# Optimization experiments

Hardware: AMD Instinct MI355X
Metric: run time of the kernel (lower is better)

## Reference

```python
import jax, jax.numpy as jnp
import numpy as np

D = 512   # word_dim
H = 4     # heads
NEG = -1.0e9


def setup_inputs() -> dict:
    key = jax.random.key(0)
    ks = jax.random.split(key, 9)
    B, N, K = 4, 1024, 32
    neibor_embedding = jax.random.normal(ks[0], (B, N, K, D), dtype=jnp.float32)
    x = jax.random.normal(ks[1], (B, N, D), dtype=jnp.float32)
    mask = jax.random.randint(ks[2], (B, N, K), 0, 2, dtype=jnp.int32)
    s = 1.0 / np.sqrt(D)
    Wq = jax.random.normal(ks[3], (D, D), dtype=jnp.float32) * s
    bq = jax.random.normal(ks[4], (D,), dtype=jnp.float32) * s
    Wk = jax.random.normal(ks[5], (D, D), dtype=jnp.float32) * s
    bk = jax.random.normal(ks[6], (D,), dtype=jnp.float32) * s
    Wv = jax.random.normal(ks[7], (D, D), dtype=jnp.float32) * s
    bv = jax.random.normal(ks[8], (D,), dtype=jnp.float32) * s
    return {"neibor_embedding": neibor_embedding, "mask": mask, "x": x,
            "Wq": Wq, "bq": bq, "Wk": Wk, "bk": bk, "Wv": Wv, "bv": bv}


def reference(neibor_embedding, mask, x, Wq, bq, Wk, bk, Wv, bv):
    B, N, K, Dm = neibor_embedding.shape
    dh = Dm // H
    # torch Linear: y = x @ W.T + b
    q = x @ Wq.T + bq                        # [B, N, D]
    k = neibor_embedding @ Wk.T + bk         # [B, N, K, D]
    v = neibor_embedding @ Wv.T + bv         # [B, N, K, D]
    q = q.reshape(B, N, H, dh)
    k = k.reshape(B, N, K, H, dh)
    v = v.reshape(B, N, K, H, dh)
    # broadcast q*k sum over head_dim -> scores [B, N, H, K] (no 1/sqrt(d) scaling, per source)
    scores = jnp.einsum('bnhd,bnkhd->bnhk', q, k)
    m = (mask[:, :, None, :] == 0)           # [B, N, 1, K] broadcasts over heads
    scores = jnp.where(m, NEG, scores)
    attn = jax.nn.softmax(scores, axis=3)    # [B, N, H, K]
    vec = jnp.einsum('bnhk,bnkhd->bnhd', attn, v)  # [B, N, H, dh]
    return vec.reshape(B, N, Dm)
```

## Files before the change

### kernel.cpp

```cpp
#include <hip/hip_runtime.h>

#define DD   512
#define KK_N 32
#define HH   4
#define DH   128
#define BN_TOT 4096

typedef __bf16 bf16x8 __attribute__((ext_vector_type(8)));
typedef float  f32x4  __attribute__((ext_vector_type(4)));
typedef unsigned short u16;

__device__ __forceinline__ unsigned rne_bf16(float x) {
    unsigned u = __float_as_uint(x);
    return (u + 0x7fffu + ((u >> 16) & 1u)) >> 16;
}
__device__ __forceinline__ float bf16_f(unsigned h16) {
    return __uint_as_float(h16 << 16);
}

__global__ __launch_bounds__(256)
void cvt3(const float4* __restrict__ s0, u16* __restrict__ h0, u16* __restrict__ l0, int n0,
          const float4* __restrict__ s1, u16* __restrict__ h1, u16* __restrict__ l1, int n1,
          const float4* __restrict__ s2, u16* __restrict__ h2, u16* __restrict__ l2, int n2)
{
    int i = blockIdx.x * 256 + threadIdx.x;
    const float4* s; u16* ph; u16* pl;
    if (i < n0)                { s = s0; ph = h0; pl = l0; }
    else if (i < n0 + n1)      { i -= n0;      s = s1; ph = h1; pl = l1; }
    else if (i < n0 + n1 + n2) { i -= n0 + n1; s = s2; ph = h2; pl = l2; }
    else return;
    float4 v = s[i];
    unsigned a = rne_bf16(v.x), b = rne_bf16(v.y), c = rne_bf16(v.z), d = rne_bf16(v.w);
    float lx = v.x - bf16_f(a), ly = v.y - bf16_f(b);
    float lz = v.z - bf16_f(c), lw = v.w - bf16_f(d);
    *(uint2*)&ph[(long)i * 4] = make_uint2(a | (b << 16), c | (d << 16));
    *(uint2*)&pl[(long)i * 4] = make_uint2(rne_bf16(lx) | (rne_bf16(ly) << 16),
                                           rne_bf16(lz) | (rne_bf16(lw) << 16));
}

__global__ __launch_bounds__(256)
void prep_wkT(const float* __restrict__ Wk, u16* __restrict__ WkTh, u16* __restrict__ WkTl)
{
    __shared__ float tile[32][DH + 1];
    const int h = blockIdx.y, o0 = blockIdx.x * 32, t = threadIdx.x;
#pragma unroll
    for (int r = 0; r < 16; r++) {
        int k = (t >> 5) + r * 8;
        tile[t & 31][k] = Wk[(long)(h * DH + k) * DD + o0 + (t & 31)];
    }
    __syncthreads();
#pragma unroll
    for (int r = 0; r < 16; r++) {
        int ol = (t >> 7) + r * 2;
        int k  = t & 127;
        float v = tile[ol][k];
        unsigned hb = rne_bf16(v);
        long o = ((long)h * DD + o0 + ol) * DH + k;
        WkTh[o] = (u16)hb;
        WkTl[o] = (u16)rne_bf16(v - bf16_f(hb));
    }
}

template<int BM, int BN>
__global__ __launch_bounds__(256)
void gemm_pre(const u16* __restrict__ Ah, const u16* __restrict__ Al, int lda, long sA,
              const u16* __restrict__ Bh, const u16* __restrict__ Bl, int ldb, long sB,
              float* __restrict__ Cf, int ldc, long sC,
              u16* __restrict__ Ch, u16* __restrict__ Cl, int ldch, long sCh,
              const float* __restrict__ bias, int sBias, int Kd)
{
    constexpr int BK  = 64;
    constexpr int LDW = 2 * BK + 8;
    constexpr int AL = BM / 32;
    constexpr int BL = BN / 32;
    constexpr int WM = BM / 2, WN = BN / 2;
    constexpr int MI = WM / 16, NI = WN / 16;

    const int z = blockIdx.z;
    Ah += (long)z * sA;  Al += (long)z * sA;
    Bh += (long)z * sB;  Bl += (long)z * sB;
    if (Cf)   Cf += (long)z * sC;
    if (Ch) { Ch += (long)z * sCh; Cl += (long)z * sCh; }
    if (bias) bias += (long)z * sBias;

    __shared__ __align__(16) u16 As[BM * LDW];
    __shared__ __align__(16) u16 Bs[BN * LDW];

    const int t    = threadIdx.x;
    const int lane = t & 63;
    const int wave = t >> 6;
    const int wm   = wave >> 1, wn = wave & 1;
    const int rbase = blockIdx.y * BM;
    const int obase = blockIdx.x * BN;

    uint4 avh[AL], avl[AL], bvh[BL], bvl[BL];
    auto loadAB = [&](int k0) {
#pragma unroll
        for (int i = 0; i < AL; i++) {
            int s = t + i * 256, kg = s & 7, row = s >> 3;
            long off = (long)(rbase + row) * lda + k0 + kg * 8;
            avh[i] = *(const uint4*)&Ah[off];
            avl[i] = *(const uint4*)&Al[off];
        }
#pragma unroll
        for (int i = 0; i < BL; i++) {
            int s = t + i * 256, kg = s & 7, row = s >> 3;
            long off = (long)(obase + row) * ldb + k0 + kg * 8;
            bvh[i] = *(const uint4*)&Bh[off];
            bvl[i] = *(const uint4*)&Bl[off];
        }
    };

    f32x4 acc[MI][NI];
#pragma unroll
    for (int m = 0; m < MI; m++)
#pragma unroll
        for (int n = 0; n < NI; n++)
            acc[m][n] = (f32x4){0.f, 0.f, 0.f, 0.f};

    const int a_base = (wm * WM + (lane & 15)) * LDW + (lane >> 4) * 16;
    const int b_base = (wn * WN + (lane & 15)) * LDW + (lane >> 4) * 16;

    loadAB(0);
    for (int k0 = 0; k0 < Kd; k0 += BK) {
        __syncthreads();
#pragma unroll
        for (int i = 0; i < AL; i++) {
            int s = t + i * 256, kg = s & 7, row = s >> 3;
            int off = row * LDW + kg * 16;
            *(uint4*)&As[off]     = avh[i];
            *(uint4*)&As[off + 8] = avl[i];
        }
#pragma unroll
        for (int i = 0; i < BL; i++) {
            int s = t + i * 256, kg = s & 7, row = s >> 3;
            int off = row * LDW + kg * 16;
            *(uint4*)&Bs[off]     = bvh[i];
            *(uint4*)&Bs[off + 8] = bvl[i];
        }
        __syncthreads();
        if (k0 + BK < Kd) loadAB(k0 + BK);

#pragma unroll
        for (int ks = 0; ks < 2; ks++) {
            bf16x8 ah[MI], al[MI], bh[NI], bl[NI];
#pragma unroll
            for (int m = 0; m < MI; m++) {
                ah[m] = *(const bf16x8*)&As[a_base + m * 16 * LDW + ks * 64];
                al[m] = *(const bf16x8*)&As[a_base + m * 16 * LDW + ks * 64 + 8];
            }
#pragma unroll
            for (int n = 0; n < NI; n++) {
                bh[n] = *(const bf16x8*)&Bs[b_base + n * 16 * LDW + ks * 64];
                bl[n] = *(const bf16x8*)&Bs[b_base + n * 16 * LDW + ks * 64 + 8];
            }
#pragma unroll
            for (int m = 0; m < MI; m++)
#pragma unroll
                for (int n = 0; n < NI; n++)
                    acc[m][n] = __builtin_amdgcn_mfma_f32_16x16x32_bf16(ah[m], bh[n], acc[m][n], 0, 0, 0);
#pragma unroll
            for (int m = 0; m < MI; m++)
#pragma unroll
                for (int n = 0; n < NI; n++)
                    acc[m][n] = __builtin_amdgcn_mfma_f32_16x16x32_bf16(ah[m], bl[n], acc[m][n], 0, 0, 0);
#pragma unroll
            for (int m = 0; m < MI; m++)
#pragma unroll
                for (int n = 0; n < NI; n++)
                    acc[m][n] = __builtin_amdgcn_mfma_f32_16x16x32_bf16(al[m], bh[n], acc[m][n], 0, 0, 0);
        }
    }

#pragma unroll
    for (int n = 0; n < NI; n++) {
        int col = obase + wn * WN + n * 16 + (lane & 15);
        float bv_ = bias ? bias[col] : 0.f;
#pragma unroll
        for (int m = 0; m < MI; m++) {
            int row0 = rbase + wm * WM + m * 16 + (lane >> 4) * 4;
#pragma unroll
            for (int j = 0; j < 4; j++) {
                float val = acc[m][n][j] + bv_;
                if (Cf) Cf[(long)(row0 + j) * ldc + col] = val;
                if (Ch) {
                    unsigned hb = rne_bf16(val);
                    long o = (long)(row0 + j) * ldch + col;
                    Ch[o] = (u16)hb;
                    Cl[o] = (u16)rne_bf16(val - bf16_f(hb));
                }
            }
        }
    }
}

__global__ __launch_bounds__(256)
void attn_fused(const float* __restrict__ ne,
                const int*   __restrict__ mask,
                const u16*   __restrict__ qh,
                const u16*   __restrict__ ql,
                const float* __restrict__ g,
                const float* __restrict__ bk,
                u16* __restrict__ wh,
                u16* __restrict__ wl)
{
    const int bn   = blockIdx.x;
    const int t    = threadIdx.x;
    const int wave = t >> 6;
    const int lane = t & 63;

    __shared__ __align__(16) float ne_s[16][516];
    __shared__ __align__(16) float g_s[HH * DD];
    __shared__ float part[4][16][HH];
    __shared__ float p_s[HH][16];
    __shared__ float c_s[HH];
    __shared__ float m_s[HH], l_s[HH], alpha_s[HH];

    {
        const float4* gs = (const float4*)(g + (long)bn * (HH * DD));
        float4 v0 = gs[t];
        float4 v1 = gs[t + 256];
        *(float4*)&g_s[t * 4]         = v0;
        *(float4*)&g_s[(t + 256) * 4] = v1;
    }
    {
        long qoff = (long)bn * DD + wave * DH + lane * 2;
        unsigned uh = *(const unsigned*)&qh[qoff];
        unsigned ul = *(const unsigned*)&ql[qoff];
        float qx = __uint_as_float(uh << 16) + __uint_as_float(ul << 16);
        float qy = __uint_as_float(uh & 0xffff0000u) + __uint_as_float(ul & 0xffff0000u);
        float2 b2 = *(const float2*)&bk[wave * DH + lane * 2];
        float cp = qx * b2.x + qy * b2.y;
#pragma unroll
        for (int off = 32; off >= 1; off >>= 1)
            cp += __shfl_xor(cp, off, 64);
        if (lane == 0) c_s[wave] = cp;
    }
    if (t < HH) { m_s[t] = -__builtin_inff(); l_s[t] = 0.f; }

    float wacc[8] = {};
    const int h_own = t >> 6;
    const int dlo   = (t & 63) * 4;
    const int kk    = t & 15;
    const int rep   = t >> 4;

    for (int ch = 0; ch < 2; ch++) {
        __syncthreads();
        {
            const float4* src = (const float4*)(ne + (long)bn * (KK_N * DD) + ch * (16 * DD));
#pragma unroll
            for (int i = 0; i < 8; i++) {
                int f = i * 256 + t;
                float4 v = src[f];
                *(float4*)&ne_s[f >> 7][(f & 127) * 4] = v;
            }
        }
        __syncthreads();
        {
            float acc[HH] = {};
#pragma unroll
            for (int i = 0; i < 8; i++) {
                float4 nv = *(const float4*)&ne_s[kk][rep * 32 + i * 4];
#pragma unroll
                for (int h = 0; h < HH; h++) {
                    float4 gv = *(const float4*)&g_s[h * DD + rep * 32 + i * 4];
                    acc[h] = fmaf(nv.x, gv.x, acc[h]);
                    acc[h] = fmaf(nv.y, gv.y, acc[h]);
                    acc[h] = fmaf(nv.z, gv.z, acc[h]);
                    acc[h] = fmaf(nv.w, gv.w, acc[h]);
                }
            }
#pragma unroll
            for (int h = 0; h < HH; h++) {
                acc[h] += __shfl_xor(acc[h], 16, 64);
                acc[h] += __shfl_xor(acc[h], 32, 64);
            }
            if ((t & 48) == 0) {
#pragma unroll
                for (int h = 0; h < HH; h++) part[wave][kk][h] = acc[h];
            }
        }
        __syncthreads();
        if (t < 64) {
            int k_i = t & 15, h = t >> 4;
            float s = part[0][k_i][h] + part[1][k_i][h] + part[2][k_i][h]
                    + part[3][k_i][h] + c_s[h];
            if (mask[(long)bn * KK_N + ch * 16 + k_i] == 0) s = -1.0e9f;
            float mx = s;
#pragma unroll
            for (int off = 8; off >= 1; off >>= 1)
                mx = fmaxf(mx, __shfl_xor(mx, off, 64));
            float m_old = m_s[h];
            float m_new = fmaxf(m_old, mx);
            float p = expf(s - m_new);
            float sm = p;
#pragma unroll
            for (int off = 8; off >= 1; off >>= 1)
                sm += __shfl_xor(sm, off, 64);
            p_s[h][k_i] = p;
            if (k_i == 0) {
                float alpha = expf(m_old - m_new);
                alpha_s[h] = alpha;
                l_s[h] = l_s[h] * alpha + sm;
                m_s[h] = m_new;
            }
        }
        __syncthreads();
        {
            float alpha = alpha_s[h_own];
#pragma unroll
            for (int j = 0; j < 8; j++) wacc[j] *= alpha;
#pragma unroll
            for (int k2 = 0; k2 < 16; k2++) {
                float pk = p_s[h_own][k2];
                float4 n0 = *(const float4*)&ne_s[k2][dlo];
                float4 n1 = *(const float4*)&ne_s[k2][256 + dlo];
                wacc[0] = fmaf(pk, n0.x, wacc[0]);
                wacc[1] = fmaf(pk, n0.y, wacc[1]);
                wacc[2] = fmaf(pk, n0.z, wacc[2]);
                wacc[3] = fmaf(pk, n0.w, wacc[3]);
                wacc[4] = fmaf(pk, n1.x, wacc[4]);
                wacc[5] = fmaf(pk, n1.y, wacc[5]);
                wacc[6] = fmaf(pk, n1.z, wacc[6]);
                wacc[7] = fmaf(pk, n1.w, wacc[7]);
            }
        }
    }
    float rl = 1.0f / l_s[h_own];
    long b0 = (long)bn * (HH * DD) + h_own * DD + dlo;
    unsigned hw[8], lw[8];
#pragma unroll
    for (int j = 0; j < 8; j++) {
        float val = wacc[j] * rl;
        hw[j] = rne_bf16(val);
        lw[j] = rne_bf16(val - bf16_f(hw[j]));
    }
    *(uint2*)&wh[b0]       = make_uint2(hw[0] | (hw[1] << 16), hw[2] | (hw[3] << 16));
    *(uint2*)&wl[b0]       = make_uint2(lw[0] | (lw[1] << 16), lw[2] | (lw[3] << 16));
    *(uint2*)&wh[b0 + 256] = make_uint2(hw[4] | (hw[5] << 16), hw[6] | (hw[7] << 16));
    *(uint2*)&wl[b0 + 256] = make_uint2(lw[4] | (lw[5] << 16), lw[6] | (lw[7] << 16));
}

extern "C" void kernel_launch(void* const* d_in, const int* in_sizes, int n_in,
                              void* d_out, int out_size, void* d_ws, size_t ws_size,
                              hipStream_t stream) {
    (void)in_sizes; (void)n_in; (void)out_size; (void)ws_size;
    const float* ne  = (const float*)d_in[0];
    const int*   msk = (const int*)  d_in[1];
    const float* x   = (const float*)d_in[2];
    const float* Wq  = (const float*)d_in[3];
    const float* bq  = (const float*)d_in[4];
    const float* Wk  = (const float*)d_in[5];
    const float* bk  = (const float*)d_in[6];
    const float* Wv  = (const float*)d_in[7];
    const float* bv  = (const float*)d_in[8];
    float* out = (float*)d_out;

    const long NQ = (long)BN_TOT * DD;
    const long NW = (long)DD * DD;
    const long NG = (long)BN_TOT * HH * DD;

    char* ws = (char*)d_ws;
    u16* xh   = (u16*)ws;              ws += NQ * 2;
    u16* xl   = (u16*)ws;              ws += NQ * 2;
    u16* wqh  = (u16*)ws;              ws += NW * 2;
    u16* wql  = (u16*)ws;              ws += NW * 2;
    u16* wvh  = (u16*)ws;              ws += NW * 2;
    u16* wvl  = (u16*)ws;              ws += NW * 2;
    u16* wkTh = (u16*)ws;              ws += NW * 2;
    u16* wkTl = (u16*)ws;              ws += NW * 2;
    u16* qh   = (u16*)ws;              ws += NQ * 2;
    u16* ql   = (u16*)ws;              ws += NQ * 2;
    u16* wneh = (u16*)ws;              ws += NG * 2;
    u16* wnel = (u16*)ws;              ws += NG * 2;
    float* g_ws = (float*)ws;

    dim3 blk(256);
    const int n4x = (int)(NQ / 4), n4w = (int)(NW / 4);
    cvt3<<<dim3((n4x + 2 * n4w) / 256), blk, 0, stream>>>(
        (const float4*)x,  xh,  xl,  n4x,
        (const float4*)Wq, wqh, wql, n4w,
        (const float4*)Wv, wvh, wvl, n4w);
    prep_wkT<<<dim3(16, HH), blk, 0, stream>>>(Wk, wkTh, wkTl);
    gemm_pre<64, 128><<<dim3(DD / 128, BN_TOT / 64, 1), blk, 0, stream>>>(
        xh, xl, DD, 0, wqh, wql, DD, 0,
        nullptr, 0, 0, qh, ql, DD, 0, bq, 0, DD);
    gemm_pre<64, 128><<<dim3(DD / 128, BN_TOT / 64, HH), blk, 0, stream>>>(
        qh, ql, DD, DH, wkTh, wkTl, DH, (long)DD * DH,
        g_ws, HH * DD, DD, nullptr, nullptr, 0, 0, nullptr, 0, DH);
    attn_fused<<<dim3(BN_TOT), blk, 0, stream>>>(ne, msk, qh, ql, g_ws, bk, wneh, wnel);
    gemm_pre<64, 128><<<dim3(1, BN_TOT / 64, HH), blk, 0, stream>>>(
        wneh, wnel, HH * DD, DD, wvh, wvl, DD, (long)DH * DD,
        out, DD, DH, nullptr, nullptr, 0, 0, bv, DH, DD);
}
```

Before: 514.5 us.

## Fuse Q projection with per-head Wk GEMM and merge prep kernels

Merges the conversion and Wk-transpose prep kernels into one launch. Adds a qg_fused kernel that computes the per-head Q tile into LDS, then multiplies it by the transposed Wk to produce g directly, and also computes the q·bk bias term into a small c_ws buffer. This removes the q round-trip through global memory and two launches. The final V GEMM tile height drops from 64 to 32 rows to raise the block count. The risk is lower per-block parallelism in the fused GEMM (32-row tiles, sequential loop over output tiles) and heavier LDS usage.

```diff
diff --git a/kernel.cpp b/kernel.cpp
--- a/kernel.cpp
+++ b/kernel.cpp
@@ -19,30 +19,30 @@
 }
 
 __global__ __launch_bounds__(256)
-void cvt3(const float4* __restrict__ s0, u16* __restrict__ h0, u16* __restrict__ l0, int n0,
-          const float4* __restrict__ s1, u16* __restrict__ h1, u16* __restrict__ l1, int n1,
-          const float4* __restrict__ s2, u16* __restrict__ h2, u16* __restrict__ l2, int n2)
-{
-    int i = blockIdx.x * 256 + threadIdx.x;
-    const float4* s; u16* ph; u16* pl;
-    if (i < n0)                { s = s0; ph = h0; pl = l0; }
-    else if (i < n0 + n1)      { i -= n0;      s = s1; ph = h1; pl = l1; }
-    else if (i < n0 + n1 + n2) { i -= n0 + n1; s = s2; ph = h2; pl = l2; }
-    else return;
-    float4 v = s[i];
-    unsigned a = rne_bf16(v.x), b = rne_bf16(v.y), c = rne_bf16(v.z), d = rne_bf16(v.w);
-    float lx = v.x - bf16_f(a), ly = v.y - bf16_f(b);
-    float lz = v.z - bf16_f(c), lw = v.w - bf16_f(d);
-    *(uint2*)&ph[(long)i * 4] = make_uint2(a | (b << 16), c | (d << 16));
-    *(uint2*)&pl[(long)i * 4] = make_uint2(rne_bf16(lx) | (rne_bf16(ly) << 16),
-                                           rne_bf16(lz) | (rne_bf16(lw) << 16));
-}
-
-__global__ __launch_bounds__(256)
-void prep_wkT(const float* __restrict__ Wk, u16* __restrict__ WkTh, u16* __restrict__ WkTl)
+void prep(const float4* __restrict__ x,  u16* __restrict__ xh,  u16* __restrict__ xl,
+          const float4* __restrict__ Wq, u16* __restrict__ wqh, u16* __restrict__ wql,
+          const float4* __restrict__ Wv, u16* __restrict__ wvh, u16* __restrict__ wvl,
+          const float*  __restrict__ Wk, u16* __restrict__ wkTh, u16* __restrict__ wkTl)
 {
     __shared__ float tile[32][DH + 1];
-    const int h = blockIdx.y, o0 = blockIdx.x * 32, t = threadIdx.x;
+    const int b = blockIdx.x, t = threadIdx.x;
+    if (b < 2560) {
+        int i = b * 256 + t;
+        const float4* s; u16* ph; u16* pl;
+        if (i < 524288)      { s = x;  ph = xh;  pl = xl;  }
+        else if (i < 589824) { i -= 524288; s = Wq; ph = wqh; pl = wql; }
+        else                 { i -= 589824; s = Wv; ph = wvh; pl = wvl; }
+        float4 v = s[i];
+        unsigned a = rne_bf16(v.x), bb = rne_bf16(v.y), c = rne_bf16(v.z), d = rne_bf16(v.w);
+        float lx = v.x - bf16_f(a), ly = v.y - bf16_f(bb);
+        float lz = v.z - bf16_f(c), lw = v.w - bf16_f(d);
+        *(uint2*)&ph[(long)i * 4] = make_uint2(a | (bb << 16), c | (d << 16));
+        *(uint2*)&pl[(long)i * 4] = make_uint2(rne_bf16(lx) | (rne_bf16(ly) << 16),
+                                               rne_bf16(lz) | (rne_bf16(lw) << 16));
+        return;
+    }
+    const int tb = b - 2560;
+    const int h = tb >> 4, o0 = (tb & 15) * 32;
 #pragma unroll
     for (int r = 0; r < 16; r++) {
         int k = (t >> 5) + r * 8;
@@ -56,8 +56,199 @@
         float v = tile[ol][k];
         unsigned hb = rne_bf16(v);
         long o = ((long)h * DD + o0 + ol) * DH + k;
-        WkTh[o] = (u16)hb;
-        WkTl[o] = (u16)rne_bf16(v - bf16_f(hb));
+        wkTh[o] = (u16)hb;
+        wkTl[o] = (u16)rne_bf16(v - bf16_f(hb));
+    }
+}
+
+__global__ __launch_bounds__(256)
+void qg_fused(const u16* __restrict__ xh,  const u16* __restrict__ xl,
+              const u16* __restrict__ wqh, const u16* __restrict__ wql,
+              const u16* __restrict__ wkTh, const u16* __restrict__ wkTl,
+              const float* __restrict__ bq, const float* __restrict__ bk,
+              float* __restrict__ g, float* __restrict__ c_ws)
+{
+    constexpr int LDW = 2 * 64 + 8;
+    constexpr int LDQ = 2 * 128 + 8;
+
+    const int h  = blockIdx.y;
+    const int r0 = blockIdx.x * 32;
+
+    __shared__ __align__(16) u16 As[32 * LDW];
+    __shared__ __align__(16) u16 Bs[128 * LDW];
+    __shared__ __align__(16) u16 q_s[32 * LDQ];
+
+    const int t = threadIdx.x, lane = t & 63, wn = t >> 6;
+
+    const int abase = (lane & 15) * LDW + (lane >> 4) * 16;
+    const int bbase = (wn * 32 + (lane & 15)) * LDW + (lane >> 4) * 16;
+
+    uint4 avh, avl, bvh[4], bvl[4];
+    auto load1 = [&](int k0) {
+        { int kg = t & 7, row = t >> 3;
+          long o = (long)(r0 + row) * DD + k0 + kg * 8;
+          avh = *(const uint4*)&xh[o]; avl = *(const uint4*)&xl[o]; }
+#pragma unroll
+        for (int i = 0; i < 4; i++) {
+            int s = t + i * 256, kg = s & 7, row = s >> 3;
+            long o = (long)(h * DH + row) * DD + k0 + kg * 8;
+            bvh[i] = *(const uint4*)&wqh[o]; bvl[i] = *(const uint4*)&wql[o];
+        }
+    };
+
+    f32x4 acc[2][2];
+#pragma unroll
+    for (int m = 0; m < 2; m++)
+#pragma unroll
+        for (int n = 0; n < 2; n++) acc[m][n] = (f32x4){0.f, 0.f, 0.f, 0.f};
+
+    load1(0);
+    for (int k0 = 0; k0 < DD; k0 += 64) {
+        __syncthreads();
+        { int kg = t & 7, row = t >> 3, off = row * LDW + kg * 16;
+          *(uint4*)&As[off] = avh; *(uint4*)&As[off + 8] = avl; }
+#pragma unroll
+        for (int i = 0; i < 4; i++) {
+            int s = t + i * 256, kg = s & 7, row = s >> 3, off = row * LDW + kg * 16;
+            *(uint4*)&Bs[off] = bvh[i]; *(uint4*)&Bs[off + 8] = bvl[i];
+        }
+        __syncthreads();
+        if (k0 + 64 < DD) load1(k0 + 64);
+#pragma unroll
+        for (int ks = 0; ks < 2; ks++) {
+            bf16x8 ah[2], al[2], bh[2], bl[2];
+#pragma unroll
+            for (int m = 0; m < 2; m++) {
+                ah[m] = *(const bf16x8*)&As[abase + m * 16 * LDW + ks * 64];
+                al[m] = *(const bf16x8*)&As[abase + m * 16 * LDW + ks * 64 + 8];
+            }
+#pragma unroll
+            for (int n = 0; n < 2; n++) {
+                bh[n] = *(const bf16x8*)&Bs[bbase + n * 16 * LDW + ks * 64];
+                bl[n] = *(const bf16x8*)&Bs[bbase + n * 16 * LDW + ks * 64 + 8];
+            }
+#pragma unroll
+            for (int m = 0; m < 2; m++)
+#pragma unroll
+                for (int n = 0; n < 2; n++)
+                    acc[m][n] = __builtin_amdgcn_mfma_f32_16x16x32_bf16(ah[m], bh[n], acc[m][n], 0, 0, 0);
+#pragma unroll
+            for (int m = 0; m < 2; m++)
+#pragma unroll
+                for (int n = 0; n < 2; n++)
+                    acc[m][n] = __builtin_amdgcn_mfma_f32_16x16x32_bf16(ah[m], bl[n], acc[m][n], 0, 0, 0);
+#pragma unroll
+            for (int m = 0; m < 2; m++)
+#pragma unroll
+                for (int n = 0; n < 2; n++)
+                    acc[m][n] = __builtin_amdgcn_mfma_f32_16x16x32_bf16(al[m], bh[n], acc[m][n], 0, 0, 0);
+        }
+    }
+#pragma unroll
+    for (int m = 0; m < 2; m++)
+#pragma unroll
+        for (int n = 0; n < 2; n++) {
+            int col = wn * 32 + n * 16 + (lane & 15);
+            float bqv = bq[h * DH + col];
+#pragma unroll
+            for (int j = 0; j < 4; j++) {
+                int row = m * 16 + (lane >> 4) * 4 + j;
+                float val = acc[m][n][j] + bqv;
+                unsigned hb = rne_bf16(val);
+                int off = row * LDQ + (col >> 3) * 16 + (col & 7);
+                q_s[off]     = (u16)hb;
+                q_s[off + 8] = (u16)rne_bf16(val - bf16_f(hb));
+            }
+        }
+    __syncthreads();
+
+    {
+        int row = t >> 3, ksl = (t & 7) * 16;
+        float sum = 0.f;
+#pragma unroll
+        for (int kk = 0; kk < 16; kk++) {
+            int k = ksl + kk;
+            int off = row * LDQ + (k >> 3) * 16 + (k & 7);
+            float qv = bf16_f(q_s[off]) + bf16_f(q_s[off + 8]);
+            sum = fmaf(qv, bk[h * DH + k], sum);
+        }
+        sum += __shfl_xor(sum, 1, 64);
+        sum += __shfl_xor(sum, 2, 64);
+        sum += __shfl_xor(sum, 4, 64);
+        if ((t & 7) == 0) c_ws[(long)(r0 + row) * HH + h] = sum;
+    }
+
+    f32x4 acc2[2][2];
+#pragma unroll
+    for (int m = 0; m < 2; m++)
+#pragma unroll
+        for (int n = 0; n < 2; n++) acc2[m][n] = (f32x4){0.f, 0.f, 0.f, 0.f};
+
+    auto load2 = [&](int it) {
+        int nt = it >> 1, k0 = (it & 1) * 64;
+#pragma unroll
+        for (int i = 0; i < 4; i++) {
+            int s = t + i * 256, kg = s & 7, row = s >> 3;
+            long o = (long)h * (DD * DH) + (long)(nt * 128 + row) * DH + k0 + kg * 8;
+            bvh[i] = *(const uint4*)&wkTh[o]; bvl[i] = *(const uint4*)&wkTl[o];
+        }
+    };
+    load2(0);
+    for (int it = 0; it < 8; it++) {
+        int nt = it >> 1, k0f = (it & 1) * 64;
+        __syncthreads();
+#pragma unroll
+        for (int i = 0; i < 4; i++) {
+            int s = t + i * 256, kg = s & 7, row = s >> 3, off = row * LDW + kg * 16;
+            *(uint4*)&Bs[off] = bvh[i]; *(uint4*)&Bs[off + 8] = bvl[i];
+        }
+        __syncthreads();
+        if (it + 1 < 8) load2(it + 1);
+#pragma unroll
+        for (int ks = 0; ks < 2; ks++) {
+            int gk = ((k0f + ks * 32) >> 3);
+            bf16x8 ah[2], al[2], bh[2], bl[2];
+#pragma unroll
+            for (int m = 0; m < 2; m++) {
+                int off = (m * 16 + (lane & 15)) * LDQ + (gk + (lane >> 4)) * 16;
+                ah[m] = *(const bf16x8*)&q_s[off];
+                al[m] = *(const bf16x8*)&q_s[off + 8];
+            }
+#pragma unroll
+            for (int n = 0; n < 2; n++) {
+                bh[n] = *(const bf16x8*)&Bs[bbase + n * 16 * LDW + ks * 64];
+                bl[n] = *(const bf16x8*)&Bs[bbase + n * 16 * LDW + ks * 64 + 8];
+            }
+#pragma unroll
+            for (int m = 0; m < 2; m++)
+#pragma unroll
+                for (int n = 0; n < 2; n++)
+                    acc2[m][n] = __builtin_amdgcn_mfma_f32_16x16x32_bf16(ah[m], bh[n], acc2[m][n], 0, 0, 0);
+#pragma unroll
+            for (int m = 0; m < 2; m++)
+#pragma unroll
+                for (int n = 0; n < 2; n++)
+                    acc2[m][n] = __builtin_amdgcn_mfma_f32_16x16x32_bf16(ah[m], bl[n], acc2[m][n], 0, 0, 0);
+#pragma unroll
+            for (int m = 0; m < 2; m++)
+#pragma unroll
+                for (int n = 0; n < 2; n++)
+                    acc2[m][n] = __builtin_amdgcn_mfma_f32_16x16x32_bf16(al[m], bh[n], acc2[m][n], 0, 0, 0);
+        }
+        if (it & 1) {
+#pragma unroll
+            for (int m = 0; m < 2; m++)
+#pragma unroll
+                for (int n = 0; n < 2; n++) {
+                    int col = nt * 128 + wn * 32 + n * 16 + (lane & 15);
+#pragma unroll
+                    for (int j = 0; j < 4; j++) {
+                        int row = m * 16 + (lane >> 4) * 4 + j;
+                        g[(long)(r0 + row) * (HH * DD) + h * DD + col] = acc2[m][n][j];
+                    }
+                    acc2[m][n] = (f32x4){0.f, 0.f, 0.f, 0.f};
+                }
+        }
     }
 }
 
@@ -197,10 +388,8 @@
 __global__ __launch_bounds__(256)
 void attn_fused(const float* __restrict__ ne,
                 const int*   __restrict__ mask,
-                const u16*   __restrict__ qh,
-                const u16*   __restrict__ ql,
+                const float* __restrict__ c_ws,
                 const float* __restrict__ g,
-                const float* __restrict__ bk,
                 u16* __restrict__ wh,
                 u16* __restrict__ wl)
 {
@@ -223,20 +412,10 @@
         *(float4*)&g_s[t * 4]         = v0;
         *(float4*)&g_s[(t + 256) * 4] = v1;
     }
-    {
-        long qoff = (long)bn * DD + wave * DH + lane * 2;
-        unsigned uh = *(const unsigned*)&qh[qoff];
-        unsigned ul = *(const unsigned*)&ql[qoff];
-        float qx = __uint_as_float(uh << 16) + __uint_as_float(ul << 16);
-        float qy = __uint_as_float(uh & 0xffff0000u) + __uint_as_float(ul & 0xffff0000u);
-        float2 b2 = *(const float2*)&bk[wave * DH + lane * 2];
-        float cp = qx * b2.x + qy * b2.y;
-#pragma unroll
-        for (int off = 32; off >= 1; off >>= 1)
-            cp += __shfl_xor(cp, off, 64);
-        if (lane == 0) c_s[wave] = cp;
-    }
-    if (t < HH) { m_s[t] = -__builtin_inff(); l_s[t] = 0.f; }
+    if (t < HH) {
+        c_s[t] = c_ws[(long)bn * HH + t];
+        m_s[t] = -__builtin_inff(); l_s[t] = 0.f;
+    }
 
     float wacc[8] = {};
     const int h_own = t >> 6;
@@ -369,27 +548,21 @@
     u16* wvl  = (u16*)ws;              ws += NW * 2;
     u16* wkTh = (u16*)ws;              ws += NW * 2;
     u16* wkTl = (u16*)ws;              ws += NW * 2;
-    u16* qh   = (u16*)ws;              ws += NQ * 2;
-    u16* ql   = (u16*)ws;              ws += NQ * 2;
     u16* wneh = (u16*)ws;              ws += NG * 2;
     u16* wnel = (u16*)ws;              ws += NG * 2;
-    float* g_ws = (float*)ws;
+    float* g_ws = (float*)ws;          ws += NG * 4;
+    float* c_ws = (float*)ws;
 
     dim3 blk(256);
-    const int n4x = (int)(NQ / 4), n4w = (int)(NW / 4);
-    cvt3<<<dim3((n4x + 2 * n4w) / 256), blk, 0, stream>>>(
-        (const float4*)x,  xh,  xl,  n4x,
-        (const float4*)Wq, wqh, wql, n4w,
-        (const float4*)Wv, wvh, wvl, n4w);
-    prep_wkT<<<dim3(16, HH), blk, 0, stream>>>(Wk, wkTh, wkTl);
-    gemm_pre<64, 128><<<dim3(DD / 128, BN_TOT / 64, 1), blk, 0, stream>>>(
-        xh, xl, DD, 0, wqh, wql, DD, 0,
-        nullptr, 0, 0, qh, ql, DD, 0, bq, 0, DD);
-    gemm_pre<64, 128><<<dim3(DD / 128, BN_TOT / 64, HH), blk, 0, stream>>>(
-        qh, ql, DD, DH, wkTh, wkTl, DH, (long)DD * DH,
-        g_ws, HH * DD, DD, nullptr, nullptr, 0, 0, nullptr, 0, DH);
-    attn_fused<<<dim3(BN_TOT), blk, 0, stream>>>(ne, msk, qh, ql, g_ws, bk, wneh, wnel);
-    gemm_pre<64, 128><<<dim3(1, BN_TOT / 64, HH), blk, 0, stream>>>(
+    prep<<<dim3(2624), blk, 0, stream>>>(
+        (const float4*)x,  xh,  xl,
+        (const float4*)Wq, wqh, wql,
+        (const float4*)Wv, wvh, wvl,
+        Wk, wkTh, wkTl);
+    qg_fused<<<dim3(BN_TOT / 32, HH), blk, 0, stream>>>(
+        xh, xl, wqh, wql, wkTh, wkTl, bq, bk, g_ws, c_ws);
+    attn_fused<<<dim3(BN_TOT), blk, 0, stream>>>(ne, msk, c_ws, g_ws, wneh, wnel);
+    gemm_pre<32, 128><<<dim3(1, BN_TOT / 32, HH), blk, 0, stream>>>(
         wneh, wnel, HH * DD, DD, wvh, wvl, DD, (long)DH * DD,
         out, DD, DH, nullptr, nullptr, 0, 0, bv, DH, DD);
 }
```

After: 504.0 us. -2.0%, faster.
